# Performance work log

Measured on AMD Instinct MI355X. Metric: run time of the kernel, lower is better.

Reference implementation:

```python
import jax, jax.numpy as jnp
import numpy as np

B, L, F, D = 128, 64, 3072, 1024
CV, CN = 512, 1024  # verb/noun concept channels
MAX_K = (L + 7) // 8
BN_EPS = 1e-5


def setup_inputs() -> dict:
    key = jax.random.key(0)
    ks = jax.random.split(key, 24)
    s_in = 1.0 / np.sqrt(F)
    s_d = 1.0 / np.sqrt(D)
    inp = {
        'inputs': jax.random.normal(ks[0], (B, L, F), jnp.float32),
        'input_lens': jax.random.randint(ks[1], (B,), 1, L + 1, jnp.int32),
        # three level linear embeds
        'W0': jax.random.normal(ks[2], (F, D), jnp.float32) * s_in,
        'b0': jnp.zeros((D,), jnp.float32),
        'W1': jax.random.normal(ks[3], (F, D), jnp.float32) * s_in,
        'b1': jnp.zeros((D,), jnp.float32),
        'W2': jax.random.normal(ks[4], (F, D), jnp.float32) * s_in,
        'b2': jnp.zeros((D,), jnp.float32),
        # attention scorer
        'w_attn': jax.random.normal(ks[5], (D, 1), jnp.float32) * s_d,
        'b_attn': jnp.zeros((1,), jnp.float32),
        # verb classifier: Conv1d(D, CV, 3, pad=1) + BN + sigmoid
        'Kv': jax.random.normal(ks[6], (CV, D, 3), jnp.float32) * (1.0 / np.sqrt(D * 3)),
        'bv': jnp.zeros((CV,), jnp.float32),
        'g_v': jnp.ones((CV,), jnp.float32),
        'beta_v': jnp.zeros((CV,), jnp.float32),
        'mean_v': jax.random.normal(ks[7], (CV,), jnp.float32) * 0.1,
        'var_v': jax.random.uniform(ks[8], (CV,), jnp.float32, 0.5, 1.5),
        # noun classifier: Conv1d(D, CN, 1) + BN + sigmoid
        'Kn': jax.random.normal(ks[9], (CN, D, 1), jnp.float32) * s_d,
        'bn_b': jnp.zeros((CN,), jnp.float32),
        'g_n': jnp.ones((CN,), jnp.float32),
        'beta_n': jnp.zeros((CN,), jnp.float32),
        'mean_n': jax.random.normal(ks[10], (CN,), jnp.float32) * 0.1,
        'var_n': jax.random.uniform(ks[11], (CN,), jnp.float32, 0.5, 1.5),
    }
    return inp


def _conv_bn_sigmoid(x_bld, K, b, gamma, beta, mean, var, pad):
    # x_bld: (B, L, D) -> permute to NCH (B, D, L) as in torch
    x = jnp.transpose(x_bld, (0, 2, 1))
    y = jax.lax.conv_general_dilated(
        x, K, window_strides=(1,), padding=[(pad, pad)],
        dimension_numbers=('NCH', 'OIH', 'NCH'))
    y = y + b[None, :, None]
    # BatchNorm1d in eval mode (running stats)
    y = (y - mean[None, :, None]) * jax.lax.rsqrt(var + BN_EPS)[None, :, None]
    y = y * gamma[None, :, None] + beta[None, :, None]
    y = jax.nn.sigmoid(y)
    return jnp.transpose(y, (0, 2, 1))  # (B, L, C)


def _topk_mean(logits, input_lens):
    # logits: (B, L, C); per-sample top-ceil(len/8) over time, then mean
    lens = input_lens.astype(jnp.int32)
    kk = (lens + 7) // 8  # (B,)
    valid = (jnp.arange(L)[None, :] < lens[:, None])  # (B, L)
    masked = jnp.where(valid[:, :, None], logits, -1e18)
    # top MAX_K per (batch, class) over time
    top = jax.lax.top_k(jnp.transpose(masked, (0, 2, 1)), MAX_K)[0]  # (B, C, MAX_K)
    take = (jnp.arange(MAX_K)[None, None, :] < kk[:, None, None]).astype(logits.dtype)
    return jnp.sum(top * take, axis=-1) / kk[:, None].astype(logits.dtype)  # (B, C)


def reference(inputs, input_lens, W0, b0, W1, b1, W2, b2, w_attn, b_attn,
              Kv, bv, g_v, beta_v, mean_v, var_v,
              Kn, bn_b, g_n, beta_n, mean_n, var_n):
    # level embeds (dropout is identity in eval)
    e0 = inputs @ W0 + b0
    e1 = inputs @ W1 + b1
    e2 = inputs @ W2 + b2

    # masked softmax attention pooling over time -> sent_embeds
    scores = (e0 @ w_attn)[:, :, 0] + b_attn[0]  # (B, L)
    valid = jnp.arange(L)[None, :] < input_lens[:, None]
    scores = jnp.where(valid, scores, -1e18)
    attn = jax.nn.softmax(scores, axis=1)
    sent_embeds = jnp.sum(e0 * attn[:, :, None], axis=1)  # (B, D)

    logits_verb = _conv_bn_sigmoid(e1, Kv, bv, g_v, beta_v, mean_v, var_v, pad=1)  # (B, L, CV)
    logits_noun = _conv_bn_sigmoid(e2, Kn, bn_b, g_n, beta_n, mean_n, var_n, pad=0)  # (B, L, CN)

    instance_logits_verb = _topk_mean(logits_verb, input_lens)  # (B, CV)
    instance_logits_noun = _topk_mean(logits_noun, input_lens)  # (B, CN)

    return (sent_embeds, e1, e2, instance_logits_verb, instance_logits_noun)
```

## Files before the change

kernel.cpp:

```cpp
#include <hip/hip_runtime.h>
#include <cstdint>
#include <cstddef>

typedef unsigned short u16;
typedef __attribute__((ext_vector_type(8))) short short8;
typedef __attribute__((ext_vector_type(4))) float f32x4;

static __device__ __forceinline__ float bf2f(u16 h) {
  union { unsigned u; float f; } a; a.u = ((unsigned)h) << 16; return a.f;
}
static __device__ __forceinline__ u16 f2bf(float x) {
  union { float f; unsigned u; } a; a.f = x;
  return (u16)((a.u + 0x7fffu + ((a.u >> 16) & 1u)) >> 16);
}

#define GLDS16(gp, lp)                                                          \
  __builtin_amdgcn_global_load_lds(                                             \
      (const __attribute__((address_space(1))) void*)(gp),                      \
      (__attribute__((address_space(3))) void*)(lp), 16, 0, 0)

__global__ void prep_all(const float* __restrict__ inputs, u16* __restrict__ Xbf,
                         const float* __restrict__ W0, const float* __restrict__ W1,
                         const float* __restrict__ W2, u16* __restrict__ Wt,
                         const float* __restrict__ Kv, const float* __restrict__ bv,
                         const float* __restrict__ g_v, const float* __restrict__ beta_v,
                         const float* __restrict__ mean_v, const float* __restrict__ var_v,
                         u16* __restrict__ KVt, float* __restrict__ biasv,
                         const float* __restrict__ Kn, const float* __restrict__ bnb,
                         const float* __restrict__ g_n, const float* __restrict__ beta_n,
                         const float* __restrict__ mean_n, const float* __restrict__ var_n,
                         u16* __restrict__ KNt, float* __restrict__ biasn,
                         u16* __restrict__ e1pad) {
  __shared__ float tile[32][33];
  const int id = blockIdx.x;
  const int tid = threadIdx.x;
  if (id < 24576) {
    const int i = id * 256 + tid;
    float4 v = ((const float4*)inputs)[i];
    ushort4 o;
    o.x = f2bf(v.x); o.y = f2bf(v.y); o.z = f2bf(v.z); o.w = f2bf(v.w);
    ((ushort4*)Xbf)[i] = o;
  } else if (id < 33792) {
    const int idd = id - 24576;
    const int kb = (idd % 96) * 32;
    const int jb = (idd / 96) * 32;
    const int tx = tid & 31, ty = tid >> 5;
    const int w = jb >> 10;
    const float* W = (w == 0) ? W0 : ((w == 1) ? W1 : W2);
    const int nb = jb & 1023;
    for (int i = ty; i < 32; i += 8)
      tile[i][tx] = W[(size_t)(kb + i) * 1024 + nb + tx];
    __syncthreads();
    for (int i = ty; i < 32; i += 8)
      Wt[(size_t)(jb + i) * 3072 + kb + tx] = f2bf(tile[tx][i]);
  } else if (id < 34304) {
    const int c = id - 33792;
    const float scale = g_v[c] * rsqrtf(var_v[c] + 1e-5f);
    for (int t = 0; t < 3; t++)
      for (int d = tid; d < 1024; d += 256)
        KVt[(size_t)c * 3072 + t * 1024 + d] = f2bf(Kv[(size_t)c * 3072 + d * 3 + t] * scale);
    if (tid == 0) biasv[c] = (bv[c] - mean_v[c]) * scale + beta_v[c];
  } else if (id < 35328) {
    const int c = id - 34304;
    const float scale = g_n[c] * rsqrtf(var_n[c] + 1e-5f);
    for (int d = tid; d < 1024; d += 256)
      KNt[(size_t)c * 1024 + d] = f2bf(Kn[(size_t)c * 1024 + d] * scale);
    if (tid == 0) biasn[c] = (bnb[c] - mean_n[c]) * scale + beta_n[c];
  } else {
    const int i = (id - 35328) * 256 + tid;
    const int b = i >> 11;
    const int j = i & 2047;
    const int r = (j < 1024) ? 0 : 65;
    const int d = j & 1023;
    e1pad[(size_t)(b * 66 + r) * 1024 + d] = 0;
  }
}

__global__ void gemm_embed(const u16* __restrict__ A, const u16* __restrict__ Bmat,
                           const float* __restrict__ bias0, const float* __restrict__ bias1,
                           const float* __restrict__ bias2,
                           float* __restrict__ oute1, float* __restrict__ oute2,
                           u16* __restrict__ e0bf, u16* __restrict__ e1pad,
                           u16* __restrict__ e2bf) {
  constexpr int K = 3072;
  __shared__ __align__(16) u16 As[128 * 32];
  __shared__ __align__(16) u16 Bs[128 * 32];

  const int tid = threadIdx.x;
  const int m0 = blockIdx.y * 128;
  const int n0 = blockIdx.x * 128;

  const int srow = tid >> 2;
  const int qlog = ((tid & 3) - (srow >> 1)) & 3;
  const int sq = qlog * 8;

  const u16* aR0 = A + (size_t)(m0 + srow) * 3072;
  const u16* aR1 = A + (size_t)(m0 + 64 + srow) * 3072;
  const u16* bR0 = Bmat + (size_t)(n0 + srow) * 3072;
  const u16* bR1 = Bmat + (size_t)(n0 + 64 + srow) * 3072;

  u16* ldsA0 = &As[tid * 8];
  u16* ldsA1 = &As[tid * 8 + 2048];
  u16* ldsB0 = &Bs[tid * 8];
  u16* ldsB1 = &Bs[tid * 8 + 2048];

  const int lane = tid & 63;
  const int warp = tid >> 6;
  const int wm = warp & 1, wn = warp >> 1;
  const int l15 = lane & 15, quad = lane >> 4;
  const int swz = (quad + (l15 >> 1)) & 3;

  const u16* aF = &As[(wm * 64 + l15) * 32 + swz * 8];
  const u16* bF = &Bs[(wn * 64 + l15) * 32 + swz * 8];

  f32x4 acc[4][4];
#pragma unroll
  for (int i = 0; i < 4; i++)
#pragma unroll
    for (int j = 0; j < 4; j++) acc[i][j] = (f32x4){0.f, 0.f, 0.f, 0.f};

  for (int k0 = 0; k0 < K; k0 += 32) {
    __syncthreads();
    GLDS16(aR0 + k0 + sq, ldsA0);
    GLDS16(aR1 + k0 + sq, ldsA1);
    GLDS16(bR0 + k0 + sq, ldsB0);
    GLDS16(bR1 + k0 + sq, ldsB1);
    __syncthreads();

    short8 fa[4], fb[4];
#pragma unroll
    for (int i = 0; i < 4; i++) fa[i] = *(const short8*)(aF + i * 512);
#pragma unroll
    for (int j = 0; j < 4; j++) fb[j] = *(const short8*)(bF + j * 512);
#pragma unroll
    for (int i = 0; i < 4; i++)
#pragma unroll
      for (int j = 0; j < 4; j++)
        acc[i][j] = __builtin_amdgcn_mfma_f32_16x16x32_bf16(fa[i], fb[j], acc[i][j], 0, 0, 0);
  }

  const int w = n0 >> 10;
  const float* bp = (w == 0) ? bias0 : ((w == 1) ? bias1 : bias2);
#pragma unroll
  for (int i = 0; i < 4; i++) {
    const int mrow = m0 + wm * 64 + i * 16 + quad * 4;
#pragma unroll
    for (int j = 0; j < 4; j++) {
      const int c = n0 + wn * 64 + j * 16 + l15;
      const int n = c & 1023;
      const float bias = bp[n];
#pragma unroll
      for (int r = 0; r < 4; r++) {
        const int m = mrow + r;
        const float v = acc[i][j][r] + bias;
        if (w == 0) {
          e0bf[(size_t)m * 1024 + n] = f2bf(v);
        } else if (w == 1) {
          oute1[(size_t)m * 1024 + n] = v;
          const int bb = m >> 6, ll = m & 63;
          e1pad[(size_t)(bb * 66 + ll + 1) * 1024 + n] = f2bf(v);
        } else {
          oute2[(size_t)m * 1024 + n] = v;
          e2bf[(size_t)m * 1024 + n] = f2bf(v);
        }
      }
    }
  }
}

template<int MODE>
__device__ __forceinline__ void conv_gemm_body(
    int bx, int by, const u16* __restrict__ A, const u16* __restrict__ Bmat,
    const float* __restrict__ bias, const int* __restrict__ lens,
    float* __restrict__ out, u16* As, u16* Bs) {
  constexpr int K = (MODE == 1) ? 3072 : 1024;
  constexpr int ldB = (MODE == 1) ? 3072 : 1024;
  constexpr int NC = (MODE == 1) ? 512 : 1024;

  const int tid = threadIdx.x;
  const int m0 = by * 128;
  const int n0 = bx * 128;

  const int srow = tid >> 2;
  const int qlog = ((tid & 3) - (srow >> 1)) & 3;
  const int sq = qlog * 8;

  const u16* aR0;
  const u16* aR1;
  int rb0 = 0, rb1 = 0;
  if constexpr (MODE == 1) {
    const int bb = m0 >> 6;
    rb0 = (bb * 66 + srow) * 1024;
    rb1 = ((bb + 1) * 66 + srow) * 1024;
    aR0 = A; aR1 = A;
  } else {
    aR0 = A + (size_t)(m0 + srow) * 1024;
    aR1 = A + (size_t)(m0 + 64 + srow) * 1024;
  }
  const u16* bR0 = Bmat + (size_t)(n0 + srow) * ldB;
  const u16* bR1 = Bmat + (size_t)(n0 + 64 + srow) * ldB;

  u16* ldsA0 = &As[tid * 8];
  u16* ldsA1 = &As[tid * 8 + 2048];
  u16* ldsB0 = &Bs[tid * 8];
  u16* ldsB1 = &Bs[tid * 8 + 2048];

  const int lane = tid & 63;
  const int warp = tid >> 6;
  const int wm = warp & 1, wn = warp >> 1;
  const int l15 = lane & 15, quad = lane >> 4;
  const int swz = (quad + (l15 >> 1)) & 3;

  const u16* aF = &As[(wm * 64 + l15) * 32 + swz * 8];
  const u16* bF = &Bs[(wn * 64 + l15) * 32 + swz * 8];

  f32x4 acc[4][4];
#pragma unroll
  for (int i = 0; i < 4; i++)
#pragma unroll
    for (int j = 0; j < 4; j++) acc[i][j] = (f32x4){0.f, 0.f, 0.f, 0.f};

  for (int k0 = 0; k0 < K; k0 += 32) {
    __syncthreads();
    const u16 *ga0, *ga1;
    if constexpr (MODE == 1) {
      const int t = k0 >> 10;
      const int kk = (k0 & 1023) + sq;
      ga0 = A + rb0 + t * 1024 + kk;
      ga1 = A + rb1 + t * 1024 + kk;
    } else {
      ga0 = aR0 + k0 + sq;
      ga1 = aR1 + k0 + sq;
    }
    GLDS16(ga0, ldsA0);
    GLDS16(ga1, ldsA1);
    GLDS16(bR0 + k0 + sq, ldsB0);
    GLDS16(bR1 + k0 + sq, ldsB1);
    __syncthreads();

    short8 fa[4], fb[4];
#pragma unroll
    for (int i = 0; i < 4; i++) fa[i] = *(const short8*)(aF + i * 512);
#pragma unroll
    for (int j = 0; j < 4; j++) fb[j] = *(const short8*)(bF + j * 512);
#pragma unroll
    for (int i = 0; i < 4; i++)
#pragma unroll
      for (int j = 0; j < 4; j++)
        acc[i][j] = __builtin_amdgcn_mfma_f32_16x16x32_bf16(fa[i], fb[j], acc[i][j], 0, 0, 0);
  }

  const int b = (m0 >> 6) + wm;
  const int len = lens[b];
  const int kk8 = (len + 7) >> 3;
#pragma unroll
  for (int j = 0; j < 4; j++) {
    const int c = n0 + wn * 64 + j * 16 + l15;
    const float bias_c = bias[c];
    float t[8];
#pragma unroll
    for (int q8 = 0; q8 < 8; q8++) t[q8] = -1e30f;
#pragma unroll
    for (int i = 0; i < 4; i++) {
#pragma unroll
      for (int r = 0; r < 4; r++) {
        const int l = i * 16 + quad * 4 + r;
        const float v = acc[i][j][r] + bias_c;
        const float sg = 1.0f / (1.0f + __expf(-v));
        float x = (l < len) ? sg : -1e30f;
#pragma unroll
        for (int q8 = 0; q8 < 8; q8++) {
          const float hi = fmaxf(t[q8], x);
          x = fminf(t[q8], x);
          t[q8] = hi;
        }
      }
    }
#pragma unroll
    for (int mask = 16; mask <= 32; mask <<= 1) {
      float xs[8];
#pragma unroll
      for (int q8 = 0; q8 < 8; q8++) xs[q8] = __shfl_xor(t[q8], mask);
#pragma unroll
      for (int q8 = 0; q8 < 8; q8++) {
        float x = xs[q8];
#pragma unroll
        for (int p8 = 0; p8 < 8; p8++) {
          const float hi = fmaxf(t[p8], x);
          x = fminf(t[p8], x);
          t[p8] = hi;
        }
      }
    }
    if (quad == 0) {
      float s = 0.f;
#pragma unroll
      for (int q8 = 0; q8 < 8; q8++) s += (q8 < kk8) ? t[q8] : 0.f;
      out[(size_t)b * NC + c] = s / (float)kk8;
    }
  }
}

__global__ void fused_tail(const u16* __restrict__ e1pad, const u16* __restrict__ KVt,
                           const float* __restrict__ biasv,
                           const u16* __restrict__ e2bf, const u16* __restrict__ KNt,
                           const float* __restrict__ biasn,
                           const u16* __restrict__ e0bf, const float* __restrict__ w_attn,
                           const float* __restrict__ b_attn, const int* __restrict__ lens,
                           float* __restrict__ out_sent, float* __restrict__ out_ilv,
                           float* __restrict__ out_iln) {
  __shared__ __align__(16) u16 smem[2 * 128 * 32 + 256];
  u16* As = smem;
  u16* Bs = smem + 128 * 32;
  const int id = blockIdx.x;
  if (id < 256) {
    conv_gemm_body<1>(id & 3, id >> 2, e1pad, KVt, biasv, lens, out_ilv, As, Bs);
  } else if (id < 768) {
    const int id2 = id - 256;
    conv_gemm_body<2>(id2 & 7, id2 >> 3, e2bf, KNt, biasn, lens, out_iln, As, Bs);
  } else {
    const int b = id - 768;
    const int tid = threadIdx.x;
    const int lane = tid & 63;
    const int warp = tid >> 6;
    float* sc = (float*)smem;
    float* at = sc + 64;
    const int len = lens[b];
    for (int t = 0; t < 16; t++) {
      const int l = warp * 16 + t;
      const u16* row = e0bf + (size_t)(b * 64 + l) * 1024;
      float s = 0.f;
#pragma unroll
      for (int u = 0; u < 16; u++) {
        const int d = lane + u * 64;
        s += bf2f(row[d]) * w_attn[d];
      }
#pragma unroll
      for (int off = 32; off > 0; off >>= 1) s += __shfl_down(s, off);
      if (lane == 0) sc[l] = s + b_attn[0];
    }
    __syncthreads();
    if (warp == 0) {
      float v = (lane < len) ? sc[lane] : -1e30f;
      float m = v;
#pragma unroll
      for (int off = 32; off > 0; off >>= 1) m = fmaxf(m, __shfl_xor(m, off));
      float p = (lane < len) ? __expf(v - m) : 0.f;
      float ssum = p;
#pragma unroll
      for (int off = 32; off > 0; off >>= 1) ssum += __shfl_xor(ssum, off);
      at[lane] = p / ssum;
    }
    __syncthreads();
    const int d0 = tid * 4;
    float a0 = 0.f, a1 = 0.f, a2 = 0.f, a3 = 0.f;
    for (int l = 0; l < 64; l++) {
      const float wgt = at[l];
      const ushort4 u4 = *(const ushort4*)(e0bf + (size_t)(b * 64 + l) * 1024 + d0);
      a0 += wgt * bf2f(u4.x);
      a1 += wgt * bf2f(u4.y);
      a2 += wgt * bf2f(u4.z);
      a3 += wgt * bf2f(u4.w);
    }
    float4 o; o.x = a0; o.y = a1; o.z = a2; o.w = a3;
    *(float4*)(out_sent + (size_t)b * 1024 + d0) = o;
  }
}

extern "C" void kernel_launch(void* const* d_in, const int* in_sizes, int n_in,
                              void* d_out, int out_size, void* d_ws, size_t ws_size,
                              hipStream_t stream) {
  const float* inputs = (const float*)d_in[0];
  const int*   lens   = (const int*)d_in[1];
  const float* W0 = (const float*)d_in[2];
  const float* b0 = (const float*)d_in[3];
  const float* W1 = (const float*)d_in[4];
  const float* b1 = (const float*)d_in[5];
  const float* W2 = (const float*)d_in[6];
  const float* b2 = (const float*)d_in[7];
  const float* w_attn = (const float*)d_in[8];
  const float* b_attn = (const float*)d_in[9];
  const float* Kv   = (const float*)d_in[10];
  const float* bv   = (const float*)d_in[11];
  const float* g_v  = (const float*)d_in[12];
  const float* beta_v = (const float*)d_in[13];
  const float* mean_v = (const float*)d_in[14];
  const float* var_v  = (const float*)d_in[15];
  const float* Kn   = (const float*)d_in[16];
  const float* bn_b = (const float*)d_in[17];
  const float* g_n  = (const float*)d_in[18];
  const float* beta_n = (const float*)d_in[19];
  const float* mean_n = (const float*)d_in[20];
  const float* var_n  = (const float*)d_in[21];

  float* out = (float*)d_out;
  float* out_sent = out;
  float* out_e1   = out + 131072;
  float* out_e2   = out + 131072 + 8388608;
  float* out_ilv  = out + 131072 + 2 * 8388608;
  float* out_iln  = out_ilv + 65536;

  char* p = (char*)d_ws;
  u16* Xbf  = (u16*)p; p += (size_t)8192 * 3072 * 2;
  u16* Wt   = (u16*)p; p += (size_t)3072 * 3072 * 2;
  u16* KVt  = (u16*)p; p += (size_t)512 * 3072 * 2;
  u16* KNt  = (u16*)p; p += (size_t)1024 * 1024 * 2;
  float* biasv = (float*)p; p += 512 * 4;
  float* biasn = (float*)p; p += 1024 * 4;
  u16* e0bf  = (u16*)p; p += (size_t)8192 * 1024 * 2;
  u16* e1pad = (u16*)p; p += (size_t)128 * 66 * 1024 * 2;
  u16* e2bf  = (u16*)p; p += (size_t)8192 * 1024 * 2;

  prep_all<<<36352, 256, 0, stream>>>(inputs, Xbf, W0, W1, W2, Wt,
                                      Kv, bv, g_v, beta_v, mean_v, var_v, KVt, biasv,
                                      Kn, bn_b, g_n, beta_n, mean_n, var_n, KNt, biasn,
                                      e1pad);
  gemm_embed<<<dim3(24, 64), 256, 0, stream>>>(Xbf, Wt, b0, b1, b2, out_e1, out_e2,
                                               e0bf, e1pad, e2bf);
  fused_tail<<<896, 256, 0, stream>>>(e1pad, KVt, biasv, e2bf, KNt, biasn,
                                      e0bf, w_attn, b_attn, lens,
                                      out_sent, out_ilv, out_iln);
}
```

Before: 515.6 us.

## Double K-step to 64 with XOR-swizzled LDS and per-batch conv tiles

The embed GEMM now stages 64-wide K slices per barrier pair using an XOR swizzle, halving the number of synchronisations per output tile. The conv/topk GEMMs switch from 128-row tiles (two batches) to 64-row tiles (one batch), with each warp covering 32 columns, which doubles the tail grid for better occupancy. LDS use per block rises, and the smaller tail tiles reload B more often.

```diff
diff --git a/kernel.cpp b/kernel.cpp
--- a/kernel.cpp
+++ b/kernel.cpp
@@ -83,35 +83,40 @@
                            u16* __restrict__ e0bf, u16* __restrict__ e1pad,
                            u16* __restrict__ e2bf) {
   constexpr int K = 3072;
-  __shared__ __align__(16) u16 As[128 * 32];
-  __shared__ __align__(16) u16 Bs[128 * 32];
+  __shared__ __align__(16) u16 As[128 * 64];
+  __shared__ __align__(16) u16 Bs[128 * 64];
 
   const int tid = threadIdx.x;
   const int m0 = blockIdx.y * 128;
   const int n0 = blockIdx.x * 128;
 
-  const int srow = tid >> 2;
-  const int qlog = ((tid & 3) - (srow >> 1)) & 3;
-  const int sq = qlog * 8;
-
-  const u16* aR0 = A + (size_t)(m0 + srow) * 3072;
-  const u16* aR1 = A + (size_t)(m0 + 64 + srow) * 3072;
-  const u16* bR0 = Bmat + (size_t)(n0 + srow) * 3072;
-  const u16* bR1 = Bmat + (size_t)(n0 + 64 + srow) * 3072;
-
-  u16* ldsA0 = &As[tid * 8];
-  u16* ldsA1 = &As[tid * 8 + 2048];
-  u16* ldsB0 = &Bs[tid * 8];
-  u16* ldsB1 = &Bs[tid * 8 + 2048];
+  const u16* aSrc[4];
+  const u16* bSrc[4];
+#pragma unroll
+  for (int i = 0; i < 4; i++) {
+    const int c = tid + i * 256;
+    const int row = c >> 3;
+    const int q = (c & 7) ^ (row & 7);
+    aSrc[i] = A + (size_t)(m0 + row) * 3072 + q * 8;
+    bSrc[i] = Bmat + (size_t)(n0 + row) * 3072 + q * 8;
+  }
 
   const int lane = tid & 63;
   const int warp = tid >> 6;
   const int wm = warp & 1, wn = warp >> 1;
   const int l15 = lane & 15, quad = lane >> 4;
-  const int swz = (quad + (l15 >> 1)) & 3;
-
-  const u16* aF = &As[(wm * 64 + l15) * 32 + swz * 8];
-  const u16* bF = &Bs[(wn * 64 + l15) * 32 + swz * 8];
+
+  const u16* aF[2][4];
+  const u16* bF[2][4];
+#pragma unroll
+  for (int s = 0; s < 2; s++)
+#pragma unroll
+    for (int i = 0; i < 4; i++) {
+      const int ra = wm * 64 + i * 16 + l15;
+      const int rb = wn * 64 + i * 16 + l15;
+      aF[s][i] = &As[ra * 64 + ((s * 4 + quad) ^ (ra & 7)) * 8];
+      bF[s][i] = &Bs[rb * 64 + ((s * 4 + quad) ^ (rb & 7)) * 8];
+    }
 
   f32x4 acc[4][4];
 #pragma unroll
@@ -119,24 +124,27 @@
 #pragma unroll
     for (int j = 0; j < 4; j++) acc[i][j] = (f32x4){0.f, 0.f, 0.f, 0.f};
 
-  for (int k0 = 0; k0 < K; k0 += 32) {
-    __syncthreads();
-    GLDS16(aR0 + k0 + sq, ldsA0);
-    GLDS16(aR1 + k0 + sq, ldsA1);
-    GLDS16(bR0 + k0 + sq, ldsB0);
-    GLDS16(bR1 + k0 + sq, ldsB1);
-    __syncthreads();
-
-    short8 fa[4], fb[4];
-#pragma unroll
-    for (int i = 0; i < 4; i++) fa[i] = *(const short8*)(aF + i * 512);
-#pragma unroll
-    for (int j = 0; j < 4; j++) fb[j] = *(const short8*)(bF + j * 512);
-#pragma unroll
-    for (int i = 0; i < 4; i++)
-#pragma unroll
-      for (int j = 0; j < 4; j++)
-        acc[i][j] = __builtin_amdgcn_mfma_f32_16x16x32_bf16(fa[i], fb[j], acc[i][j], 0, 0, 0);
+  for (int k0 = 0; k0 < K; k0 += 64) {
+    __syncthreads();
+#pragma unroll
+    for (int i = 0; i < 4; i++) GLDS16(aSrc[i] + k0, &As[(tid + i * 256) * 8]);
+#pragma unroll
+    for (int i = 0; i < 4; i++) GLDS16(bSrc[i] + k0, &Bs[(tid + i * 256) * 8]);
+    __syncthreads();
+
+#pragma unroll
+    for (int s = 0; s < 2; s++) {
+      short8 fa[4], fb[4];
+#pragma unroll
+      for (int i = 0; i < 4; i++) fa[i] = *(const short8*)aF[s][i];
+#pragma unroll
+      for (int j = 0; j < 4; j++) fb[j] = *(const short8*)bF[s][j];
+#pragma unroll
+      for (int i = 0; i < 4; i++)
+#pragma unroll
+        for (int j = 0; j < 4; j++)
+          acc[i][j] = __builtin_amdgcn_mfma_f32_16x16x32_bf16(fa[i], fb[j], acc[i][j], 0, 0, 0);
+    }
   }
 
   const int w = n0 >> 10;
@@ -172,90 +180,95 @@
 __device__ __forceinline__ void conv_gemm_body(
     int bx, int by, const u16* __restrict__ A, const u16* __restrict__ Bmat,
     const float* __restrict__ bias, const int* __restrict__ lens,
-    float* __restrict__ out, u16* As, u16* Bs) {
+    float* __restrict__ out, u16* As , u16* Bs ) {
   constexpr int K = (MODE == 1) ? 3072 : 1024;
   constexpr int ldB = (MODE == 1) ? 3072 : 1024;
   constexpr int NC = (MODE == 1) ? 512 : 1024;
 
   const int tid = threadIdx.x;
-  const int m0 = by * 128;
+  const int b = by;
   const int n0 = bx * 128;
 
-  const int srow = tid >> 2;
-  const int qlog = ((tid & 3) - (srow >> 1)) & 3;
-  const int sq = qlog * 8;
-
-  const u16* aR0;
-  const u16* aR1;
-  int rb0 = 0, rb1 = 0;
-  if constexpr (MODE == 1) {
-    const int bb = m0 >> 6;
-    rb0 = (bb * 66 + srow) * 1024;
-    rb1 = ((bb + 1) * 66 + srow) * 1024;
-    aR0 = A; aR1 = A;
-  } else {
-    aR0 = A + (size_t)(m0 + srow) * 1024;
-    aR1 = A + (size_t)(m0 + 64 + srow) * 1024;
-  }
-  const u16* bR0 = Bmat + (size_t)(n0 + srow) * ldB;
-  const u16* bR1 = Bmat + (size_t)(n0 + 64 + srow) * ldB;
-
-  u16* ldsA0 = &As[tid * 8];
-  u16* ldsA1 = &As[tid * 8 + 2048];
-  u16* ldsB0 = &Bs[tid * 8];
-  u16* ldsB1 = &Bs[tid * 8 + 2048];
+  int aRow[2], aQ[2];
+#pragma unroll
+  for (int i = 0; i < 2; i++) {
+    const int c = tid + i * 256;
+    aRow[i] = c >> 3;
+    aQ[i] = ((c & 7) ^ (aRow[i] & 7)) * 8;
+  }
+  const u16* bSrc[4];
+#pragma unroll
+  for (int i = 0; i < 4; i++) {
+    const int c = tid + i * 256;
+    const int row = c >> 3;
+    const int q = (c & 7) ^ (row & 7);
+    bSrc[i] = Bmat + (size_t)(n0 + row) * ldB + q * 8;
+  }
 
   const int lane = tid & 63;
-  const int warp = tid >> 6;
-  const int wm = warp & 1, wn = warp >> 1;
+  const int wn = tid >> 6;
   const int l15 = lane & 15, quad = lane >> 4;
-  const int swz = (quad + (l15 >> 1)) & 3;
-
-  const u16* aF = &As[(wm * 64 + l15) * 32 + swz * 8];
-  const u16* bF = &Bs[(wn * 64 + l15) * 32 + swz * 8];
-
-  f32x4 acc[4][4];
+
+  const u16* aF[2][4];
+  const u16* bF[2][2];
+#pragma unroll
+  for (int s = 0; s < 2; s++) {
+#pragma unroll
+    for (int i = 0; i < 4; i++) {
+      const int ra = i * 16 + l15;
+      aF[s][i] = &As[ra * 64 + ((s * 4 + quad) ^ (ra & 7)) * 8];
+    }
+#pragma unroll
+    for (int j = 0; j < 2; j++) {
+      const int rb = wn * 32 + j * 16 + l15;
+      bF[s][j] = &Bs[rb * 64 + ((s * 4 + quad) ^ (rb & 7)) * 8];
+    }
+  }
+
+  f32x4 acc[4][2];
 #pragma unroll
   for (int i = 0; i < 4; i++)
 #pragma unroll
-    for (int j = 0; j < 4; j++) acc[i][j] = (f32x4){0.f, 0.f, 0.f, 0.f};
-
-  for (int k0 = 0; k0 < K; k0 += 32) {
-    __syncthreads();
-    const u16 *ga0, *ga1;
-    if constexpr (MODE == 1) {
-      const int t = k0 >> 10;
-      const int kk = (k0 & 1023) + sq;
-      ga0 = A + rb0 + t * 1024 + kk;
-      ga1 = A + rb1 + t * 1024 + kk;
-    } else {
-      ga0 = aR0 + k0 + sq;
-      ga1 = aR1 + k0 + sq;
-    }
-    GLDS16(ga0, ldsA0);
-    GLDS16(ga1, ldsA1);
-    GLDS16(bR0 + k0 + sq, ldsB0);
-    GLDS16(bR1 + k0 + sq, ldsB1);
-    __syncthreads();
-
-    short8 fa[4], fb[4];
-#pragma unroll
-    for (int i = 0; i < 4; i++) fa[i] = *(const short8*)(aF + i * 512);
-#pragma unroll
-    for (int j = 0; j < 4; j++) fb[j] = *(const short8*)(bF + j * 512);
-#pragma unroll
-    for (int i = 0; i < 4; i++)
-#pragma unroll
-      for (int j = 0; j < 4; j++)
-        acc[i][j] = __builtin_amdgcn_mfma_f32_16x16x32_bf16(fa[i], fb[j], acc[i][j], 0, 0, 0);
-  }
-
-  const int b = (m0 >> 6) + wm;
+    for (int j = 0; j < 2; j++) acc[i][j] = (f32x4){0.f, 0.f, 0.f, 0.f};
+
+  for (int k0 = 0; k0 < K; k0 += 64) {
+    __syncthreads();
+#pragma unroll
+    for (int i = 0; i < 2; i++) {
+      const u16* ga;
+      if constexpr (MODE == 1) {
+        const int t = k0 >> 10;
+        const int kk = (k0 & 1023) + aQ[i];
+        ga = A + (size_t)(b * 66 + aRow[i] + t) * 1024 + kk;
+      } else {
+        ga = A + (size_t)(b * 64 + aRow[i]) * 1024 + k0 + aQ[i];
+      }
+      GLDS16(ga, &As[(tid + i * 256) * 8]);
+    }
+#pragma unroll
+    for (int i = 0; i < 4; i++) GLDS16(bSrc[i] + k0, &Bs[(tid + i * 256) * 8]);
+    __syncthreads();
+
+#pragma unroll
+    for (int s = 0; s < 2; s++) {
+      short8 fa[4], fb[2];
+#pragma unroll
+      for (int i = 0; i < 4; i++) fa[i] = *(const short8*)aF[s][i];
+#pragma unroll
+      for (int j = 0; j < 2; j++) fb[j] = *(const short8*)bF[s][j];
+#pragma unroll
+      for (int i = 0; i < 4; i++)
+#pragma unroll
+        for (int j = 0; j < 2; j++)
+          acc[i][j] = __builtin_amdgcn_mfma_f32_16x16x32_bf16(fa[i], fb[j], acc[i][j], 0, 0, 0);
+    }
+  }
+
   const int len = lens[b];
   const int kk8 = (len + 7) >> 3;
 #pragma unroll
-  for (int j = 0; j < 4; j++) {
-    const int c = n0 + wn * 64 + j * 16 + l15;
+  for (int j = 0; j < 2; j++) {
+    const int c = n0 + wn * 32 + j * 16 + l15;
     const float bias_c = bias[c];
     float t[8];
 #pragma unroll
@@ -309,17 +322,17 @@
                            const float* __restrict__ b_attn, const int* __restrict__ lens,
                            float* __restrict__ out_sent, float* __restrict__ out_ilv,
                            float* __restrict__ out_iln) {
-  __shared__ __align__(16) u16 smem[2 * 128 * 32 + 256];
+  __shared__ __align__(16) u16 smem[64 * 64 + 128 * 64];
   u16* As = smem;
-  u16* Bs = smem + 128 * 32;
+  u16* Bs = smem + 64 * 64;
   const int id = blockIdx.x;
-  if (id < 256) {
+  if (id < 512) {
     conv_gemm_body<1>(id & 3, id >> 2, e1pad, KVt, biasv, lens, out_ilv, As, Bs);
-  } else if (id < 768) {
-    const int id2 = id - 256;
+  } else if (id < 1536) {
+    const int id2 = id - 512;
     conv_gemm_body<2>(id2 & 7, id2 >> 3, e2bf, KNt, biasn, lens, out_iln, As, Bs);
   } else {
-    const int b = id - 768;
+    const int b = id - 1536;
     const int tid = threadIdx.x;
     const int lane = tid & 63;
     const int warp = tid >> 6;
@@ -417,7 +430,7 @@
                                       e1pad);
   gemm_embed<<<dim3(24, 64), 256, 0, stream>>>(Xbf, Wt, b0, b1, b2, out_e1, out_e2,
                                                e0bf, e1pad, e2bf);
-  fused_tail<<<896, 256, 0, stream>>>(e1pad, KVt, biasv, e2bf, KNt, biasn,
-                                      e0bf, w_attn, b_attn, lens,
-                                      out_sent, out_ilv, out_iln);
-}
+  fused_tail<<<1664, 256, 0, stream>>>(e1pad, KVt, biasv, e2bf, KNt, biasn,
+                                       e0bf, w_attn, b_attn, lens,
+                                       out_sent, out_ilv, out_iln);
+}
```

After: 532.6 us. 1.03x slower.
